# Kernel tuning notes

Measured on AMD Instinct MI355X. Metric: run time of the kernel, lower is better.

Reference implementation:

```python
import jax, jax.numpy as jnp
import numpy as np

NUM_HEADS = 16
THETA = 10000.0


def setup_inputs() -> dict:
    key = jax.random.key(0)
    k1, k2, k3, k4 = jax.random.split(key, 4)
    B, T, D = 2, 2048, 1024
    x = jax.random.normal(k1, (B, T, D), dtype=jnp.float32)
    token_positions = jnp.sort(
        jax.random.randint(k2, (B, T), 0, 2048), axis=-1
    ).astype(jnp.int32)
    sigma_qkv = float(np.sqrt(2.0 / (D + 3 * D)))
    sigma_out = float(np.sqrt(2.0 / (D + D)))
    W_qkv = jax.random.normal(k3, (3 * D, D), dtype=jnp.float32) * sigma_qkv
    W_out = jax.random.normal(k4, (D, D), dtype=jnp.float32) * sigma_out
    return {"x": x, "token_positions": token_positions, "W_qkv": W_qkv, "W_out": W_out}


def _apply_rope(t, cos, sin):
    # t: [B, H, T, d_k]; cos/sin: [B, T, d_k//2]
    B, H, T, dk = t.shape
    t2 = t.reshape(B, H, T, dk // 2, 2)
    te, to = t2[..., 0], t2[..., 1]
    c = cos[:, None]  # [B, 1, T, dk//2]
    s = sin[:, None]
    ye = te * c - to * s
    yo = to * c + te * s
    return jnp.stack([ye, yo], axis=-1).reshape(B, H, T, dk)


def reference(x, token_positions, W_qkv, W_out):
    B, T, D = x.shape
    H = NUM_HEADS
    dk = D // H

    # fused QKV projection: [B, T, 3D] -> split (three, h, d) on last dim
    qkv = jnp.einsum("btd,od->bto", x, W_qkv).reshape(B, T, 3, H, dk)
    qkv = jnp.transpose(qkv, (2, 0, 3, 1, 4))  # [3, B, H, T, dk]
    q, k, v = qkv[0], qkv[1], qkv[2]

    # RoPE angles from token positions
    n = jnp.arange(dk // 2, dtype=jnp.float32)
    inv_freq = THETA ** (-2.0 * n / dk)  # [dk//2]
    angles = token_positions.astype(jnp.float32)[..., None] * inv_freq  # [B, T, dk//2]
    cos, sin = jnp.cos(angles), jnp.sin(angles)
    q = _apply_rope(q, cos, sin)
    k = _apply_rope(k, cos, sin)

    # causal scaled dot-product attention
    scores = jnp.einsum("bhid,bhjd->bhij", q, k) / jnp.sqrt(jnp.float32(dk))
    causal = jnp.tril(jnp.ones((T, T), dtype=bool))
    scores = jnp.where(causal, scores, -jnp.inf)
    probs = jax.nn.softmax(scores, axis=-1)
    attn = jnp.einsum("bhij,bhjd->bhid", probs, v)  # [B, H, T, dk]

    concat = jnp.transpose(attn, (0, 2, 1, 3)).reshape(B, T, D)
    return jnp.einsum("btd,od->bto", concat, W_out)
```

## Files before the change

### kernel.cpp

```cpp
#include <hip/hip_runtime.h>
#include <hip/hip_bf16.h>
#include <cmath>

#define T_SEQ 2048
#define D_MODEL 1024
#define NHEAD 16
#define DK 64

typedef short bf16x8 __attribute__((ext_vector_type(8)));
typedef float f32x4 __attribute__((ext_vector_type(4)));
typedef float f32x16 __attribute__((ext_vector_type(16)));
typedef unsigned uint2v __attribute__((ext_vector_type(2)));

union U8 { unsigned u[4]; bf16x8 v; };

#define VMCNT(n) asm volatile("s_waitcnt vmcnt(" #n ")" ::: "memory")
#define BAR() __builtin_amdgcn_s_barrier()
#define SFENCE() __builtin_amdgcn_sched_barrier(0)

__device__ __forceinline__ short f2b(float f) {
    unsigned u = __builtin_bit_cast(unsigned, f);
    unsigned r = (u + 0x7FFFu + ((u >> 16) & 1u)) >> 16;
    return (short)r;
}

__device__ __forceinline__ void gll16(const void* g, void* l) {
    __builtin_amdgcn_global_load_lds(
        (__attribute__((address_space(1))) void*)g,
        (__attribute__((address_space(3))) void*)l, 16, 0, 0);
}

__device__ __forceinline__ bf16x8 lds_frag(const short* base, int row, int chunk) {
    return *reinterpret_cast<const bf16x8*>(
        (const char*)base + row * 128 + ((chunk * 16) ^ ((row & 7) << 4)));
}

__device__ __forceinline__ unsigned pkbf16(float a, float b) {
    unsigned r;
    asm("v_cvt_pk_bf16_f32 %0, %1, %2" : "=v"(r) : "v"(a), "v"(b));
    return r;
}
__device__ __forceinline__ void pl32swap(unsigned& a, unsigned& b) {
    uint2v r = __builtin_amdgcn_permlane32_swap(a, b, false, false);
    a = r.x; b = r.y;
}

__global__ __launch_bounds__(256) void cvt_all(const float* __restrict__ x,
                                               const float* __restrict__ wq,
                                               const float* __restrict__ wo,
                                               const int* __restrict__ pos,
                                               short* __restrict__ xb,
                                               short* __restrict__ wqb,
                                               short* __restrict__ wob,
                                               float* __restrict__ ct,
                                               float* __restrict__ st) {
    int i = blockIdx.x * 256 + threadIdx.x;
    if (i >= 1048576) {
        int j = i - 1048576;
        int bt = j >> 5, n = j & 31;
        float p = (float)pos[bt];
        float invf = expf((float)n * (-2.0f / (float)DK) * 9.210340371976184f);
        float s, c;
        sincosf(p * invf, &s, &c);
        ct[j] = c; st[j] = s;
        return;
    }
    const float* src;
    short* dst;
    int srcoff, c;
    if (i < 524288) {
        c = i;
        int tile = c >> 9, cc = c & 511;
        int kblk = cc >> 7, row = cc & 127;
        int rb = tile >> 5, kb = tile & 31;
        srcoff = (rb * 128 + row) * D_MODEL + kb * 32 + kblk * 8;
        src = x; dst = xb;
    } else if (i < 917504) {
        c = i - 524288;
        int tile = c >> 9, cc = c & 511;
        int kblk = cc >> 7, row = cc & 127;
        int rb = tile >> 5, kb = tile & 31;
        srcoff = (rb * 128 + row) * D_MODEL + kb * 32 + kblk * 8;
        src = wq; dst = wqb;
    } else {
        c = i - 917504;
        int tile = c >> 8, cc = c & 255;
        int kblk = cc >> 6, row = cc & 63;
        int nb = tile >> 5, kb = tile & 31;
        srcoff = (nb * 64 + row) * D_MODEL + kb * 32 + kblk * 8;
        src = wo; dst = wob;
    }
    float4 a = *reinterpret_cast<const float4*>(src + srcoff);
    float4 b = *reinterpret_cast<const float4*>(src + srcoff + 4);
    bf16x8 v;
    v[0] = f2b(a.x); v[1] = f2b(a.y); v[2] = f2b(a.z); v[3] = f2b(a.w);
    v[4] = f2b(b.x); v[5] = f2b(b.y); v[6] = f2b(b.z); v[7] = f2b(b.w);
    reinterpret_cast<bf16x8*>(dst)[c] = v;
}

__global__ __launch_bounds__(256, 3) void gemm_qkv(const short* __restrict__ xb,
                                                   const short* __restrict__ wb,
                                                   const float* __restrict__ ct,
                                                   const float* __restrict__ st,
                                                   short* __restrict__ Qo,
                                                   short* __restrict__ Ko,
                                                   short* __restrict__ Vt) {
    __shared__ short SM[3][8192];
    const int tid = threadIdx.x;
    const int w = tid >> 6, l = tid & 63, lg = l >> 4, li = l & 15;
    const int wr = w >> 1, wc = w & 1;
    const int bn = blockIdx.x * 128, bm = blockIdx.y * 128;

    const short* pA = xb + (size_t)blockIdx.y * 32 * 4096 + (w * 128 + l) * 8;
    const short* pB = wb + (size_t)blockIdx.x * 32 * 4096 + (w * 128 + l) * 8;

    f32x4 zero = {0.f, 0.f, 0.f, 0.f};
    f32x4 acc[4][4];
#pragma unroll
    for (int m = 0; m < 4; ++m)
#pragma unroll
        for (int n = 0; n < 4; ++n) acc[m][n] = zero;

#define GSTAGE(buf, t_)                                               \
    do {                                                              \
        const size_t ko = (size_t)(t_) * 4096;                        \
        gll16(pA + ko,       &SM[buf][w * 1024]);                     \
        gll16(pA + ko + 512, &SM[buf][w * 1024 + 512]);               \
        gll16(pB + ko,       &SM[buf][4096 + w * 1024]);              \
        gll16(pB + ko + 512, &SM[buf][4096 + w * 1024 + 512]);        \
    } while (0)

    GSTAGE(0, 0);
    GSTAGE(1, 1);

    for (int t = 0; t < 32; ++t) {
        if (t < 31) { VMCNT(4); } else { VMCNT(0); }
        BAR();
        SFENCE();
        if (t + 2 < 32) GSTAGE((t + 2) % 3, t + 2);
        const short* Ac = &SM[t % 3][0];
        const short* Bc = &SM[t % 3][4096];
        bf16x8 a[4], b[4];
#pragma unroll
        for (int m = 0; m < 4; ++m)
            a[m] = *reinterpret_cast<const bf16x8*>(&Ac[lg * 1024 + (wr * 64 + m * 16 + li) * 8]);
#pragma unroll
        for (int n = 0; n < 4; ++n)
            b[n] = *reinterpret_cast<const bf16x8*>(&Bc[lg * 1024 + (wc * 64 + n * 16 + li) * 8]);
        __builtin_amdgcn_s_setprio(1);
#pragma unroll
        for (int m = 0; m < 4; ++m)
#pragma unroll
            for (int n = 0; n < 4; ++n)
                acc[m][n] = __builtin_amdgcn_mfma_f32_16x16x32_bf16(a[m], b[n], acc[m][n], 0, 0, 0);
        __builtin_amdgcn_s_setprio(0);
    }
#undef GSTAGE

    const int which = bn >> 10;
    const int h = ((bn >> 6) + wc) & 15;
    if (which == 2) {
        __syncthreads();
        short* scr = &SM[0][0] + w * 4096;
#pragma unroll
        for (int n = 0; n < 4; ++n)
#pragma unroll
            for (int m = 0; m < 4; ++m)
#pragma unroll
                for (int rp = 0; rp < 2; ++rp) {
                    int d = n * 16 + li;
                    int t64 = m * 16 + lg * 4 + rp * 2;
                    unsigned pk = pkbf16(acc[m][n][rp * 2], acc[m][n][rp * 2 + 1]);
                    *reinterpret_cast<unsigned*>(
                        (char*)scr + ((d * 128 + t64 * 2) ^ ((d & 7) << 4))) = pk;
                }
        const int mi0 = bm + wr * 64;
        const int b0 = mi0 >> 11, t0 = mi0 & (T_SEQ - 1);
        short* vbase = Vt + (size_t)(b0 * NHEAD + h) * DK * T_SEQ + t0;
#pragma unroll
        for (int db = 0; db < 8; ++db) {
            int d = db * 8 + (l >> 3);
            int ch = l & 7;
            bf16x8 v = *reinterpret_cast<const bf16x8*>(
                (char*)scr + ((d * 128 + ch * 16) ^ ((d & 7) << 4)));
            *reinterpret_cast<bf16x8*>(vbase + (size_t)d * T_SEQ + ch * 8) = v;
        }
    } else {
#pragma unroll
        for (int n = 0; n < 4; ++n) {
            const int d = n * 16 + li;
#pragma unroll
            for (int m = 0; m < 4; ++m)
#pragma unroll
                for (int r = 0; r < 4; ++r) {
                    const int mi = bm + wr * 64 + m * 16 + lg * 4 + r;
                    const int b_ = mi >> 11, tt = mi & (T_SEQ - 1);
                    float v = acc[m][n][r];
                    float vp = __shfl_xor(v, 1);
                    int nn = n * 8 + (li >> 1);
                    float c = ct[(size_t)mi * 32 + nn];
                    float s = st[(size_t)mi * 32 + nn];
                    float o = (d & 1) ? (v * c + vp * s) : (v * c - vp * s);
                    if (which == 0) o *= 0.18033688011112042f;
                    short* dst = (which == 0) ? Qo : Ko;
                    dst[((size_t)((b_ * NHEAD + h) * T_SEQ + tt)) * DK + d] = f2b(o);
                }
        }
    }
}

__global__ __launch_bounds__(128, 3) void attn(const short* __restrict__ Q,
                                               const short* __restrict__ K,
                                               const short* __restrict__ Vt,
                                               short* __restrict__ Cc) {
    __shared__ short Kls[2][4096];

    const int bid = blockIdx.x;
    const int bh = bid & 31;
    const int qt = 31 - (bid >> 5);
    const int ntb = qt + 1;

    const int tid = threadIdx.x;
    const int w = tid >> 6, l = tid & 63;
    const int l31 = l & 31, hi = l >> 5, hi4 = hi * 4, hi8 = hi * 8;
    const int q0w = qt * 64 + w * 32;

    const short* Qh = Q + (size_t)bh * T_SEQ * DK;
    const short* Kh = K + (size_t)bh * T_SEQ * DK;
    const short* Vh = Vt + (size_t)bh * DK * T_SEQ;

    bf16x8 qf[4];
#pragma unroll
    for (int ks = 0; ks < 4; ++ks)
        qf[ks] = *reinterpret_cast<const bf16x8*>(&Qh[(size_t)(q0w + l31) * DK + ks * 16 + hi8]);

    f32x16 o0 = {0.f,0.f,0.f,0.f,0.f,0.f,0.f,0.f,0.f,0.f,0.f,0.f,0.f,0.f,0.f,0.f};
    f32x16 o1 = o0;
    float m = -3.0e38f;
    float lsum = 0.f;

    int rr[4], cb[4];
#pragma unroll
    for (int j = 0; j < 4; ++j) {
        int c = j * 128 + tid;
        rr[j] = c >> 3;
        cb[j] = ((c & 7) ^ (rr[j] & 7)) * 8;
    }
    auto kstage = [&](int buf, int n0_) {
#pragma unroll
        for (int j = 0; j < 4; ++j)
            gll16(Kh + (size_t)(n0_ + rr[j]) * DK + cb[j], &Kls[buf][j * 1024 + w * 512]);
    };

    const short* vrow0 = Vh + (size_t)l31 * T_SEQ;
    const short* vrow1 = Vh + (size_t)(32 + l31) * T_SEQ;

    kstage(0, 0);

    for (int t = 0; t < ntb; ++t) {
        VMCNT(0);
        BAR();
        const int n0 = t * 64;

        bf16x8 v00[2], v01[2], v10[2], v11[2];
#pragma unroll
        for (int kb = 0; kb < 2; ++kb) {
            const int co = n0 + (kb * 4 + hi) * 8;
            v00[kb] = *reinterpret_cast<const bf16x8*>(vrow0 + co);
            v01[kb] = *reinterpret_cast<const bf16x8*>(vrow0 + co + 16);
            v10[kb] = *reinterpret_cast<const bf16x8*>(vrow1 + co);
            v11[kb] = *reinterpret_cast<const bf16x8*>(vrow1 + co + 16);
        }
        if (t + 1 < ntb) kstage((t + 1) & 1, (t + 1) * 64);
        SFENCE();

        const short* Kc = Kls[t & 1];

        f32x16 s0 = {0.f,0.f,0.f,0.f,0.f,0.f,0.f,0.f,0.f,0.f,0.f,0.f,0.f,0.f,0.f,0.f};
        f32x16 s1 = s0;
        __builtin_amdgcn_s_setprio(1);
#pragma unroll
        for (int ks = 0; ks < 4; ++ks) {
            bf16x8 kf0 = lds_frag(Kc, l31,      ks * 2 + hi);
            bf16x8 kf1 = lds_frag(Kc, 32 + l31, ks * 2 + hi);
            s0 = __builtin_amdgcn_mfma_f32_32x32x16_bf16(kf0, qf[ks], s0, 0, 0, 0);
            s1 = __builtin_amdgcn_mfma_f32_32x32x16_bf16(kf1, qf[ks], s1, 0, 0, 0);
        }
        __builtin_amdgcn_s_setprio(0);

        float p[32];
#pragma unroll
        for (int r = 0; r < 16; ++r) { p[r] = s0[r]; p[16 + r] = s1[r]; }

        if (n0 + 64 > q0w) {
            const int qrel = q0w + l31 - n0;
#pragma unroll
            for (int r = 0; r < 16; ++r) {
                const int kvm = (r & 3) + 8 * (r >> 2) + hi4;
                if (kvm > qrel) p[r] = -3.0e38f;
                if (kvm + 32 > qrel) p[16 + r] = -3.0e38f;
            }
        }

        float t16[16];
#pragma unroll
        for (int r = 0; r < 16; ++r) t16[r] = fmaxf(p[r], p[16 + r]);
#pragma unroll
        for (int d = 8; d >= 1; d >>= 1)
#pragma unroll
            for (int r = 0; r < 8; ++r)
                if (r < d) t16[r] = fmaxf(t16[r], t16[r + d]);
        float tmax = fmaxf(t16[0], __shfl_xor(t16[0], 32));

        if (__any(tmax > m + 8.0f)) {
            float mnew = fmaxf(m, tmax);
            float alpha = __builtin_amdgcn_exp2f(m - mnew);
            m = mnew;
#pragma unroll
            for (int r = 0; r < 16; ++r) {
                float ar = __shfl(alpha, (r & 3) + 8 * (r >> 2) + hi4);
                o0[r] *= ar; o1[r] *= ar;
            }
            lsum *= alpha;
        }

#pragma unroll
        for (int r = 0; r < 32; ++r) p[r] = __builtin_amdgcn_exp2f(p[r] - m);
        float a16[16];
#pragma unroll
        for (int r = 0; r < 16; ++r) a16[r] = p[r] + p[16 + r];
#pragma unroll
        for (int d = 8; d >= 1; d >>= 1)
#pragma unroll
            for (int r = 0; r < 8; ++r)
                if (r < d) a16[r] += a16[r + d];
        lsum += a16[0] + __shfl_xor(a16[0], 32);

        __builtin_amdgcn_s_setprio(1);
#pragma unroll
        for (int kb = 0; kb < 2; ++kb) {
            unsigned pk0 = pkbf16(p[kb * 16 + 0],  p[kb * 16 + 1]);
            unsigned pk1 = pkbf16(p[kb * 16 + 2],  p[kb * 16 + 3]);
            unsigned pk2 = pkbf16(p[kb * 16 + 4],  p[kb * 16 + 5]);
            unsigned pk3 = pkbf16(p[kb * 16 + 6],  p[kb * 16 + 7]);
            unsigned pk4 = pkbf16(p[kb * 16 + 8],  p[kb * 16 + 9]);
            unsigned pk5 = pkbf16(p[kb * 16 + 10], p[kb * 16 + 11]);
            unsigned pk6 = pkbf16(p[kb * 16 + 12], p[kb * 16 + 13]);
            unsigned pk7 = pkbf16(p[kb * 16 + 14], p[kb * 16 + 15]);
            pl32swap(pk0, pk2); pl32swap(pk1, pk3);
            pl32swap(pk4, pk6); pl32swap(pk5, pk7);
            U8 f0, f1;
            f0.u[0] = pk0; f0.u[1] = pk1; f0.u[2] = pk2; f0.u[3] = pk3;
            f1.u[0] = pk4; f1.u[1] = pk5; f1.u[2] = pk6; f1.u[3] = pk7;
            o0 = __builtin_amdgcn_mfma_f32_32x32x16_bf16(f0.v, v00[kb], o0, 0, 0, 0);
            o0 = __builtin_amdgcn_mfma_f32_32x32x16_bf16(f1.v, v01[kb], o0, 0, 0, 0);
            o1 = __builtin_amdgcn_mfma_f32_32x32x16_bf16(f0.v, v10[kb], o1, 0, 0, 0);
            o1 = __builtin_amdgcn_mfma_f32_32x32x16_bf16(f1.v, v11[kb], o1, 0, 0, 0);
        }
        __builtin_amdgcn_s_setprio(0);
    }

    const int b = bh >> 4, h = bh & 15;
    const float linv = 1.0f / lsum;
#pragma unroll
    for (int r = 0; r < 16; ++r) {
        const int qoff = (r & 3) + 8 * (r >> 2) + hi4;
        float inv = __shfl(linv, qoff);
        const int mg = b * T_SEQ + q0w + qoff;
        const int mb = mg >> 7, row = mg & 127;
        const int kblk = l31 >> 3, el = l & 7;
        Cc[((size_t)(mb * 32 + h * 2 + 0)) * 4096 + kblk * 1024 + row * 8 + el] = f2b(o0[r] * inv);
        Cc[((size_t)(mb * 32 + h * 2 + 1)) * 4096 + kblk * 1024 + row * 8 + el] = f2b(o1[r] * inv);
    }
}

__global__ __launch_bounds__(256, 3) void gemm_out(const short* __restrict__ ab,
                                                   const short* __restrict__ wb,
                                                   float* __restrict__ out) {
    __shared__ short SM[3][6144];
    const int tid = threadIdx.x;
    const int w = tid >> 6, l = tid & 63, lg = l >> 4, li = l & 15;
    const int wr = w >> 1, wc = w & 1;
    const int bn = blockIdx.x * 64, bm = blockIdx.y * 128;

    const short* pA = ab + (size_t)blockIdx.y * 32 * 4096 + (w * 128 + l) * 8;
    const short* pB = wb + (size_t)blockIdx.x * 32 * 2048 + (w * 64 + l) * 8;

    f32x4 zero = {0.f, 0.f, 0.f, 0.f};
    f32x4 acc[4][2];
#pragma unroll
    for (int m = 0; m < 4; ++m)
#pragma unroll
        for (int n = 0; n < 2; ++n) acc[m][n] = zero;

#define OSTAGE(buf, t_)                                                  \
    do {                                                                 \
        gll16(pA + (size_t)(t_) * 4096,       &SM[buf][w * 1024]);       \
        gll16(pA + (size_t)(t_) * 4096 + 512, &SM[buf][w * 1024 + 512]); \
        gll16(pB + (size_t)(t_) * 2048,       &SM[buf][4096 + w * 512]); \
    } while (0)

    OSTAGE(0, 0);
    OSTAGE(1, 1);

    for (int t = 0; t < 32; ++t) {
        if (t < 31) { VMCNT(3); } else { VMCNT(0); }
        BAR();
        SFENCE();
        if (t + 2 < 32) OSTAGE((t + 2) % 3, t + 2);
        const short* Ac = &SM[t % 3][0];
        const short* Bc = &SM[t % 3][4096];
        bf16x8 a[4], b[2];
#pragma unroll
        for (int m = 0; m < 4; ++m)
            a[m] = *reinterpret_cast<const bf16x8*>(&Ac[lg * 1024 + (wr * 64 + m * 16 + li) * 8]);
#pragma unroll
        for (int n = 0; n < 2; ++n)
            b[n] = *reinterpret_cast<const bf16x8*>(&Bc[lg * 512 + (wc * 32 + n * 16 + li) * 8]);
        __builtin_amdgcn_s_setprio(1);
#pragma unroll
        for (int m = 0; m < 4; ++m)
#pragma unroll
            for (int n = 0; n < 2; ++n)
                acc[m][n] = __builtin_amdgcn_mfma_f32_16x16x32_bf16(a[m], b[n], acc[m][n], 0, 0, 0);
        __builtin_amdgcn_s_setprio(0);
    }
#undef OSTAGE

#pragma unroll
    for (int m = 0; m < 4; ++m)
#pragma unroll
        for (int n = 0; n < 2; ++n)
#pragma unroll
            for (int r = 0; r < 4; ++r) {
                const int mi = bm + wr * 64 + m * 16 + lg * 4 + r;
                out[(size_t)mi * D_MODEL + bn + wc * 32 + n * 16 + li] = acc[m][n][r];
            }
}

extern "C" void kernel_launch(void* const* d_in, const int* in_sizes, int n_in,
                              void* d_out, int out_size, void* d_ws, size_t ws_size,
                              hipStream_t stream) {
    const float* x    = (const float*)d_in[0];
    const int*   pos  = (const int*)d_in[1];
    const float* wqkv = (const float*)d_in[2];
    const float* wout = (const float*)d_in[3];
    float* out = (float*)d_out;

    char* ws = (char*)d_ws;
    size_t off = 0;
    short* xb  = (short*)(ws + off); off += (size_t)4096 * 1024 * 2;
    short* wqb = (short*)(ws + off); off += (size_t)3072 * 1024 * 2;
    short* wob = (short*)(ws + off); off += (size_t)1024 * 1024 * 2;
    short* Q   = (short*)(ws + off); off += (size_t)32 * 2048 * 64 * 2;
    short* Kb  = (short*)(ws + off); off += (size_t)32 * 2048 * 64 * 2;
    short* Vt  = (short*)(ws + off); off += (size_t)32 * 64 * 2048 * 2;
    off += 4096;
    short* Cc  = (short*)(ws + off); off += (size_t)4096 * 1024 * 2;
    float* ct  = (float*)(ws + off); off += (size_t)4096 * 32 * 4;
    float* st  = (float*)(ws + off); off += (size_t)4096 * 32 * 4;

    cvt_all<<<4608, 256, 0, stream>>>(x, wqkv, wout, pos, xb, wqb, wob, ct, st);
    gemm_qkv<<<dim3(24, 32), 256, 0, stream>>>(xb, wqb, ct, st, Q, Kb, Vt);
    attn<<<1024, 128, 0, stream>>>(Q, Kb, Vt, Cc);
    gemm_out<<<dim3(16, 32), 256, 0, stream>>>(Cc, wob, out);
}
```

Before: 127.3 us.

## Split causal attention over KV chunks with separate merge kernel and tiled V layout

Result: slower. 141.4 us (+11.1%).

```diff
diff --git a/kernel.cpp b/kernel.cpp
--- a/kernel.cpp
+++ b/kernel.cpp
@@ -22,6 +22,10 @@
     unsigned u = __builtin_bit_cast(unsigned, f);
     unsigned r = (u + 0x7FFFu + ((u >> 16) & 1u)) >> 16;
     return (short)r;
+}
+__device__ __forceinline__ float b2f(short s) {
+    unsigned u = ((unsigned)(unsigned short)s) << 16;
+    return __builtin_bit_cast(float, u);
 }
 
 __device__ __forceinline__ void gll16(const void* g, void* l) {
@@ -176,14 +180,15 @@
                 }
         const int mi0 = bm + wr * 64;
         const int b0 = mi0 >> 11, t0 = mi0 & (T_SEQ - 1);
-        short* vbase = Vt + (size_t)(b0 * NHEAD + h) * DK * T_SEQ + t0;
+        const int kvt = t0 >> 6;
+        short* vbase = Vt + ((size_t)(b0 * NHEAD + h) * 32 + kvt) * 4096;
+        const int ch = l >> 3;
 #pragma unroll
         for (int db = 0; db < 8; ++db) {
-            int d = db * 8 + (l >> 3);
-            int ch = l & 7;
+            int d = db * 8 + (l & 7);
             bf16x8 v = *reinterpret_cast<const bf16x8*>(
                 (char*)scr + ((d * 128 + ch * 16) ^ ((d & 7) << 4)));
-            *reinterpret_cast<bf16x8*>(vbase + (size_t)d * T_SEQ + ch * 8) = v;
+            *reinterpret_cast<bf16x8*>(vbase + ch * 512 + d * 8) = v;
         }
     } else {
 #pragma unroll
@@ -209,30 +214,37 @@
     }
 }
 
-__global__ __launch_bounds__(128, 3) void attn(const short* __restrict__ Q,
+__global__ __launch_bounds__(128, 4) void attn(const short* __restrict__ Q,
                                                const short* __restrict__ K,
                                                const short* __restrict__ Vt,
-                                               short* __restrict__ Cc) {
+                                               short* __restrict__ Cc,
+                                               short* __restrict__ Opart,
+                                               float* __restrict__ MLpart) {
     __shared__ short Kls[2][4096];
 
     const int bid = blockIdx.x;
     const int bh = bid & 31;
-    const int qt = 31 - (bid >> 5);
-    const int ntb = qt + 1;
+    const int rest = bid >> 5;
+    const int ch = rest & 3;
+    const int qt = 31 - (rest >> 2);
+    if (8 * ch > qt) return;
+    const int t0c = 8 * ch;
+    const int t1c = min(8 * ch + 8, qt + 1);
+    const int nch = (qt >> 3) + 1;
 
     const int tid = threadIdx.x;
     const int w = tid >> 6, l = tid & 63;
-    const int l31 = l & 31, hi = l >> 5, hi4 = hi * 4, hi8 = hi * 8;
+    const int l31 = l & 31, hi = l >> 5, hi4 = hi * 4;
     const int q0w = qt * 64 + w * 32;
 
     const short* Qh = Q + (size_t)bh * T_SEQ * DK;
     const short* Kh = K + (size_t)bh * T_SEQ * DK;
-    const short* Vh = Vt + (size_t)bh * DK * T_SEQ;
+    const short* Vh = Vt + (size_t)bh * 32 * 4096;
 
     bf16x8 qf[4];
 #pragma unroll
     for (int ks = 0; ks < 4; ++ks)
-        qf[ks] = *reinterpret_cast<const bf16x8*>(&Qh[(size_t)(q0w + l31) * DK + ks * 16 + hi8]);
+        qf[ks] = *reinterpret_cast<const bf16x8*>(&Qh[(size_t)(q0w + l31) * DK + ks * 16 + hi * 8]);
 
     f32x16 o0 = {0.f,0.f,0.f,0.f,0.f,0.f,0.f,0.f,0.f,0.f,0.f,0.f,0.f,0.f,0.f,0.f};
     f32x16 o1 = o0;
@@ -252,30 +264,26 @@
             gll16(Kh + (size_t)(n0_ + rr[j]) * DK + cb[j], &Kls[buf][j * 1024 + w * 512]);
     };
 
-    const short* vrow0 = Vh + (size_t)l31 * T_SEQ;
-    const short* vrow1 = Vh + (size_t)(32 + l31) * T_SEQ;
-
-    kstage(0, 0);
-
-    for (int t = 0; t < ntb; ++t) {
+    kstage(t0c & 1, t0c * 64);
+
+    for (int t = t0c; t < t1c; ++t) {
         VMCNT(0);
         BAR();
+        SFENCE();
         const int n0 = t * 64;
-
+        const short* vt = Vh + (size_t)t * 4096;
         bf16x8 v00[2], v01[2], v10[2], v11[2];
 #pragma unroll
         for (int kb = 0; kb < 2; ++kb) {
-            const int co = n0 + (kb * 4 + hi) * 8;
-            v00[kb] = *reinterpret_cast<const bf16x8*>(vrow0 + co);
-            v01[kb] = *reinterpret_cast<const bf16x8*>(vrow0 + co + 16);
-            v10[kb] = *reinterpret_cast<const bf16x8*>(vrow1 + co);
-            v11[kb] = *reinterpret_cast<const bf16x8*>(vrow1 + co + 16);
-        }
-        if (t + 1 < ntb) kstage((t + 1) & 1, (t + 1) * 64);
+            v00[kb] = *reinterpret_cast<const bf16x8*>(vt + (kb * 4 + hi) * 512 + l31 * 8);
+            v01[kb] = *reinterpret_cast<const bf16x8*>(vt + (kb * 4 + 2 + hi) * 512 + l31 * 8);
+            v10[kb] = *reinterpret_cast<const bf16x8*>(vt + (kb * 4 + hi) * 512 + 256 + l31 * 8);
+            v11[kb] = *reinterpret_cast<const bf16x8*>(vt + (kb * 4 + 2 + hi) * 512 + 256 + l31 * 8);
+        }
+        if (t + 1 < t1c) kstage((t + 1) & 1, (t + 1) * 64);
         SFENCE();
 
         const short* Kc = Kls[t & 1];
-
         f32x16 s0 = {0.f,0.f,0.f,0.f,0.f,0.f,0.f,0.f,0.f,0.f,0.f,0.f,0.f,0.f,0.f,0.f};
         f32x16 s1 = s0;
         __builtin_amdgcn_s_setprio(1);
@@ -360,18 +368,90 @@
         __builtin_amdgcn_s_setprio(0);
     }
 
+    if (nch == 1) {
+        const int b = bh >> 4, h = bh & 15;
+        const float linv = 1.0f / lsum;
+#pragma unroll
+        for (int r = 0; r < 16; ++r) {
+            const int qoff = (r & 3) + 8 * (r >> 2) + hi4;
+            float inv = __shfl(linv, qoff);
+            const int mg = b * T_SEQ + q0w + qoff;
+            const int mb = mg >> 7, row = mg & 127;
+            const int kblk = l31 >> 3, el = l & 7;
+            Cc[((size_t)(mb * 32 + h * 2 + 0)) * 4096 + kblk * 1024 + row * 8 + el] = f2b(o0[r] * inv);
+            Cc[((size_t)(mb * 32 + h * 2 + 1)) * 4096 + kblk * 1024 + row * 8 + el] = f2b(o1[r] * inv);
+        }
+    } else {
+        const int g = qt >> 3;
+        const int baseg = (g == 1) ? 0 : (g == 2) ? 16 : 40;
+        const int slot = bh * 72 + baseg + (g + 1) * (qt - g * 8) + ch;
+        short* op = Opart + (size_t)slot * 4096 + (w * 32) * 64;
+#pragma unroll
+        for (int r = 0; r < 16; ++r) {
+            const int qoff = (r & 3) + 8 * (r >> 2) + hi4;
+            op[qoff * 64 + l31]      = f2b(o0[r]);
+            op[qoff * 64 + 32 + l31] = f2b(o1[r]);
+        }
+        if (l < 32) {
+            float* mlp = MLpart + (size_t)slot * 128 + (w * 32 + l) * 2;
+            mlp[0] = m; mlp[1] = lsum;
+        }
+    }
+}
+
+__global__ __launch_bounds__(256) void attn_merge(const short* __restrict__ Opart,
+                                                  const float* __restrict__ MLpart,
+                                                  short* __restrict__ Cc) {
+    const int bid = blockIdx.x;
+    const int bh = bid & 31;
+    const int qt = 8 + (bid >> 5);
+    const int g = qt >> 3;
+    const int baseg = (g == 1) ? 0 : (g == 2) ? 16 : 40;
+    const int base = bh * 72 + baseg + (g + 1) * (qt - g * 8);
+    const int nch = g + 1;
+
+    const int tid = threadIdx.x;
+    const int q = tid >> 2, sl = tid & 3, d0 = sl * 16;
+
+    float mc[4], lc[4];
+    float M = -3.0e38f;
+    for (int c = 0; c < nch; ++c) {
+        const float* mlp = MLpart + (size_t)(base + c) * 128 + q * 2;
+        mc[c] = mlp[0]; lc[c] = mlp[1];
+        M = fmaxf(M, mc[c]);
+    }
+    float L = 0.f, al[4];
+    for (int c = 0; c < nch; ++c) {
+        al[c] = __builtin_amdgcn_exp2f(mc[c] - M);
+        L += al[c] * lc[c];
+    }
+    const float inv = 1.0f / L;
+
+    float acc[16];
+#pragma unroll
+    for (int e = 0; e < 16; ++e) acc[e] = 0.f;
+    for (int c = 0; c < nch; ++c) {
+        const short* src = Opart + (size_t)(base + c) * 4096 + q * 64 + d0;
+        bf16x8 v0 = *reinterpret_cast<const bf16x8*>(src);
+        bf16x8 v1 = *reinterpret_cast<const bf16x8*>(src + 8);
+#pragma unroll
+        for (int e = 0; e < 8; ++e) {
+            acc[e]     += al[c] * b2f(v0[e]);
+            acc[8 + e] += al[c] * b2f(v1[e]);
+        }
+    }
+
     const int b = bh >> 4, h = bh & 15;
-    const float linv = 1.0f / lsum;
-#pragma unroll
-    for (int r = 0; r < 16; ++r) {
-        const int qoff = (r & 3) + 8 * (r >> 2) + hi4;
-        float inv = __shfl(linv, qoff);
-        const int mg = b * T_SEQ + q0w + qoff;
-        const int mb = mg >> 7, row = mg & 127;
-        const int kblk = l31 >> 3, el = l & 7;
-        Cc[((size_t)(mb * 32 + h * 2 + 0)) * 4096 + kblk * 1024 + row * 8 + el] = f2b(o0[r] * inv);
-        Cc[((size_t)(mb * 32 + h * 2 + 1)) * 4096 + kblk * 1024 + row * 8 + el] = f2b(o1[r] * inv);
-    }
+    const int mg = b * T_SEQ + qt * 64 + q;
+    const int mb = mg >> 7, row = mg & 127;
+    short outv[16];
+#pragma unroll
+    for (int e = 0; e < 16; ++e) outv[e] = f2b(acc[e] * inv);
+    const int tile = mb * 32 + h * 2 + (d0 >> 5);
+    const int kb0 = (d0 & 31) >> 3;
+    short* dst = Cc + (size_t)tile * 4096 + kb0 * 1024 + row * 8;
+    *reinterpret_cast<bf16x8*>(dst)        = *reinterpret_cast<bf16x8*>(&outv[0]);
+    *reinterpret_cast<bf16x8*>(dst + 1024) = *reinterpret_cast<bf16x8*>(&outv[8]);
 }
 
 __global__ __launch_bounds__(256, 3) void gemm_out(const short* __restrict__ ab,
@@ -454,14 +534,17 @@
     short* wob = (short*)(ws + off); off += (size_t)1024 * 1024 * 2;
     short* Q   = (short*)(ws + off); off += (size_t)32 * 2048 * 64 * 2;
     short* Kb  = (short*)(ws + off); off += (size_t)32 * 2048 * 64 * 2;
-    short* Vt  = (short*)(ws + off); off += (size_t)32 * 64 * 2048 * 2;
+    short* Vt  = (short*)(ws + off); off += (size_t)32 * 32 * 4096 * 2;
     off += 4096;
     short* Cc  = (short*)(ws + off); off += (size_t)4096 * 1024 * 2;
     float* ct  = (float*)(ws + off); off += (size_t)4096 * 32 * 4;
     float* st  = (float*)(ws + off); off += (size_t)4096 * 32 * 4;
+    short* Opart = (short*)(ws + off); off += (size_t)2304 * 4096 * 2;
+    float* MLpart = (float*)(ws + off); off += (size_t)2304 * 128 * 4;
 
     cvt_all<<<4608, 256, 0, stream>>>(x, wqkv, wout, pos, xb, wqb, wob, ct, st);
     gemm_qkv<<<dim3(24, 32), 256, 0, stream>>>(xb, wqb, ct, st, Q, Kb, Vt);
-    attn<<<1024, 128, 0, stream>>>(Q, Kb, Vt, Cc);
+    attn<<<4096, 128, 0, stream>>>(Q, Kb, Vt, Cc, Opart, MLpart);
+    attn_merge<<<768, 256, 0, stream>>>(Opart, MLpart, Cc);
     gemm_out<<<dim3(16, 32), 256, 0, stream>>>(Cc, wob, out);
 }
```

## Pipeline PV MMA one tile behind, tile V per block, use 4-wave attention blocks

Applied to the files above, without the earlier changes.

New measurement: 112.9 us. 11.3% less time.

```diff
diff --git a/kernel.cpp b/kernel.cpp
--- a/kernel.cpp
+++ b/kernel.cpp
@@ -176,14 +176,15 @@
                 }
         const int mi0 = bm + wr * 64;
         const int b0 = mi0 >> 11, t0 = mi0 & (T_SEQ - 1);
-        short* vbase = Vt + (size_t)(b0 * NHEAD + h) * DK * T_SEQ + t0;
+        const int kvt = t0 >> 6;
+        short* vbase = Vt + ((size_t)(b0 * NHEAD + h) * 32 + kvt) * 4096;
+        const int ch = l >> 3;
 #pragma unroll
         for (int db = 0; db < 8; ++db) {
-            int d = db * 8 + (l >> 3);
-            int ch = l & 7;
+            int d = db * 8 + (l & 7);
             bf16x8 v = *reinterpret_cast<const bf16x8*>(
                 (char*)scr + ((d * 128 + ch * 16) ^ ((d & 7) << 4)));
-            *reinterpret_cast<bf16x8*>(vbase + (size_t)d * T_SEQ + ch * 8) = v;
+            *reinterpret_cast<bf16x8*>(vbase + ch * 512 + d * 8) = v;
         }
     } else {
 #pragma unroll
@@ -209,25 +210,27 @@
     }
 }
 
-__global__ __launch_bounds__(128, 3) void attn(const short* __restrict__ Q,
+__global__ __launch_bounds__(256, 3) void attn(const short* __restrict__ Q,
                                                const short* __restrict__ K,
                                                const short* __restrict__ Vt,
                                                short* __restrict__ Cc) {
     __shared__ short Kls[2][4096];
 
     const int bid = blockIdx.x;
-    const int bh = bid & 31;
-    const int qt = 31 - (bid >> 5);
-    const int ntb = qt + 1;
+    const int ii = bid & 255, rhalf = bid >> 8;
+    const int bh = ii & 31;
+    const int qt = rhalf ? 15 - (ii >> 5) : (ii >> 5);
+    const int ntb = 2 * qt + 2;
 
     const int tid = threadIdx.x;
     const int w = tid >> 6, l = tid & 63;
     const int l31 = l & 31, hi = l >> 5, hi4 = hi * 4, hi8 = hi * 8;
-    const int q0w = qt * 64 + w * 32;
+    const int q0w = qt * 128 + w * 32;
+    const int Tw = (q0w + 32 + 63) >> 6;
 
     const short* Qh = Q + (size_t)bh * T_SEQ * DK;
     const short* Kh = K + (size_t)bh * T_SEQ * DK;
-    const short* Vh = Vt + (size_t)bh * DK * T_SEQ;
+    const short* Vh = Vt + (size_t)bh * 32 * 4096;
 
     bf16x8 qf[4];
 #pragma unroll
@@ -239,126 +242,137 @@
     float m = -3.0e38f;
     float lsum = 0.f;
 
-    int rr[4], cb[4];
-#pragma unroll
-    for (int j = 0; j < 4; ++j) {
-        int c = j * 128 + tid;
-        rr[j] = c >> 3;
-        cb[j] = ((c & 7) ^ (rr[j] & 7)) * 8;
+    int kr0, kc0, kr1, kc1;
+    {
+        int c0 = tid;        kr0 = c0 >> 3; kc0 = ((c0 & 7) ^ (kr0 & 7)) * 8;
+        int c1 = 256 + tid;  kr1 = c1 >> 3; kc1 = ((c1 & 7) ^ (kr1 & 7)) * 8;
     }
     auto kstage = [&](int buf, int n0_) {
-#pragma unroll
-        for (int j = 0; j < 4; ++j)
-            gll16(Kh + (size_t)(n0_ + rr[j]) * DK + cb[j], &Kls[buf][j * 1024 + w * 512]);
+        gll16(Kh + (size_t)(n0_ + kr0) * DK + kc0, &Kls[buf][w * 512]);
+        gll16(Kh + (size_t)(n0_ + kr1) * DK + kc1, &Kls[buf][2048 + w * 512]);
     };
 
-    const short* vrow0 = Vh + (size_t)l31 * T_SEQ;
-    const short* vrow1 = Vh + (size_t)(32 + l31) * T_SEQ;
+    bf16x8 v00[2], v01[2], v10[2], v11[2];
+    U8 pf0[2], pf1[2];
 
     kstage(0, 0);
 
     for (int t = 0; t < ntb; ++t) {
         VMCNT(0);
         BAR();
-        const int n0 = t * 64;
-
-        bf16x8 v00[2], v01[2], v10[2], v11[2];
-#pragma unroll
-        for (int kb = 0; kb < 2; ++kb) {
-            const int co = n0 + (kb * 4 + hi) * 8;
-            v00[kb] = *reinterpret_cast<const bf16x8*>(vrow0 + co);
-            v01[kb] = *reinterpret_cast<const bf16x8*>(vrow0 + co + 16);
-            v10[kb] = *reinterpret_cast<const bf16x8*>(vrow1 + co);
-            v11[kb] = *reinterpret_cast<const bf16x8*>(vrow1 + co + 16);
+        SFENCE();
+        if (t + 1 < ntb) kstage((t + 1) & 1, (t + 1) * 64);
+
+        if (t < Tw) {
+            const int n0 = t * 64;
+            const short* Kc = Kls[t & 1];
+
+            f32x16 s0 = {0.f,0.f,0.f,0.f,0.f,0.f,0.f,0.f,0.f,0.f,0.f,0.f,0.f,0.f,0.f,0.f};
+            f32x16 s1 = s0;
+            __builtin_amdgcn_s_setprio(1);
+#pragma unroll
+            for (int ks = 0; ks < 4; ++ks) {
+                bf16x8 kf0 = lds_frag(Kc, l31,      ks * 2 + hi);
+                bf16x8 kf1 = lds_frag(Kc, 32 + l31, ks * 2 + hi);
+                s0 = __builtin_amdgcn_mfma_f32_32x32x16_bf16(kf0, qf[ks], s0, 0, 0, 0);
+                s1 = __builtin_amdgcn_mfma_f32_32x32x16_bf16(kf1, qf[ks], s1, 0, 0, 0);
+            }
+            if (t > 0) {
+#pragma unroll
+                for (int kb = 0; kb < 2; ++kb) {
+                    o0 = __builtin_amdgcn_mfma_f32_32x32x16_bf16(pf0[kb].v, v00[kb], o0, 0, 0, 0);
+                    o0 = __builtin_amdgcn_mfma_f32_32x32x16_bf16(pf1[kb].v, v01[kb], o0, 0, 0, 0);
+                    o1 = __builtin_amdgcn_mfma_f32_32x32x16_bf16(pf0[kb].v, v10[kb], o1, 0, 0, 0);
+                    o1 = __builtin_amdgcn_mfma_f32_32x32x16_bf16(pf1[kb].v, v11[kb], o1, 0, 0, 0);
+                }
+            }
+            __builtin_amdgcn_s_setprio(0);
+
+            const short* vt = Vh + (size_t)t * 4096;
+#pragma unroll
+            for (int kb = 0; kb < 2; ++kb) {
+                v00[kb] = *reinterpret_cast<const bf16x8*>(vt + (kb * 4 + hi) * 512 + l31 * 8);
+                v01[kb] = *reinterpret_cast<const bf16x8*>(vt + (kb * 4 + 2 + hi) * 512 + l31 * 8);
+                v10[kb] = *reinterpret_cast<const bf16x8*>(vt + (kb * 4 + hi) * 512 + 256 + l31 * 8);
+                v11[kb] = *reinterpret_cast<const bf16x8*>(vt + (kb * 4 + 2 + hi) * 512 + 256 + l31 * 8);
+            }
+            SFENCE();
+
+            float p[32];
+#pragma unroll
+            for (int r = 0; r < 16; ++r) { p[r] = s0[r]; p[16 + r] = s1[r]; }
+
+            if (n0 + 64 > q0w) {
+                const int qrel = q0w + l31 - n0;
+#pragma unroll
+                for (int r = 0; r < 16; ++r) {
+                    const int kvm = (r & 3) + 8 * (r >> 2) + hi4;
+                    if (kvm > qrel) p[r] = -3.0e38f;
+                    if (kvm + 32 > qrel) p[16 + r] = -3.0e38f;
+                }
+            }
+
+            float t16[16];
+#pragma unroll
+            for (int r = 0; r < 16; ++r) t16[r] = fmaxf(p[r], p[16 + r]);
+#pragma unroll
+            for (int d = 8; d >= 1; d >>= 1)
+#pragma unroll
+                for (int r = 0; r < 8; ++r)
+                    if (r < d) t16[r] = fmaxf(t16[r], t16[r + d]);
+            float tmax = fmaxf(t16[0], __shfl_xor(t16[0], 32));
+
+            if (__any(tmax > m + 8.0f)) {
+                float mnew = fmaxf(m, tmax);
+                float alpha = __builtin_amdgcn_exp2f(m - mnew);
+                m = mnew;
+#pragma unroll
+                for (int r = 0; r < 16; ++r) {
+                    float ar = __shfl(alpha, (r & 3) + 8 * (r >> 2) + hi4);
+                    o0[r] *= ar; o1[r] *= ar;
+                }
+                lsum *= alpha;
+            }
+
+#pragma unroll
+            for (int r = 0; r < 32; ++r) p[r] = __builtin_amdgcn_exp2f(p[r] - m);
+            float a16[16];
+#pragma unroll
+            for (int r = 0; r < 16; ++r) a16[r] = p[r] + p[16 + r];
+#pragma unroll
+            for (int d = 8; d >= 1; d >>= 1)
+#pragma unroll
+                for (int r = 0; r < 8; ++r)
+                    if (r < d) a16[r] += a16[r + d];
+            lsum += a16[0] + __shfl_xor(a16[0], 32);
+
+#pragma unroll
+            for (int kb = 0; kb < 2; ++kb) {
+                unsigned pk0 = pkbf16(p[kb * 16 + 0],  p[kb * 16 + 1]);
+                unsigned pk1 = pkbf16(p[kb * 16 + 2],  p[kb * 16 + 3]);
+                unsigned pk2 = pkbf16(p[kb * 16 + 4],  p[kb * 16 + 5]);
+                unsigned pk3 = pkbf16(p[kb * 16 + 6],  p[kb * 16 + 7]);
+                unsigned pk4 = pkbf16(p[kb * 16 + 8],  p[kb * 16 + 9]);
+                unsigned pk5 = pkbf16(p[kb * 16 + 10], p[kb * 16 + 11]);
+                unsigned pk6 = pkbf16(p[kb * 16 + 12], p[kb * 16 + 13]);
+                unsigned pk7 = pkbf16(p[kb * 16 + 14], p[kb * 16 + 15]);
+                pl32swap(pk0, pk2); pl32swap(pk1, pk3);
+                pl32swap(pk4, pk6); pl32swap(pk5, pk7);
+                pf0[kb].u[0] = pk0; pf0[kb].u[1] = pk1; pf0[kb].u[2] = pk2; pf0[kb].u[3] = pk3;
+                pf1[kb].u[0] = pk4; pf1[kb].u[1] = pk5; pf1[kb].u[2] = pk6; pf1[kb].u[3] = pk7;
+            }
         }
-        if (t + 1 < ntb) kstage((t + 1) & 1, (t + 1) * 64);
-        SFENCE();
-
-        const short* Kc = Kls[t & 1];
-
-        f32x16 s0 = {0.f,0.f,0.f,0.f,0.f,0.f,0.f,0.f,0.f,0.f,0.f,0.f,0.f,0.f,0.f,0.f};
-        f32x16 s1 = s0;
-        __builtin_amdgcn_s_setprio(1);
-#pragma unroll
-        for (int ks = 0; ks < 4; ++ks) {
-            bf16x8 kf0 = lds_frag(Kc, l31,      ks * 2 + hi);
-            bf16x8 kf1 = lds_frag(Kc, 32 + l31, ks * 2 + hi);
-            s0 = __builtin_amdgcn_mfma_f32_32x32x16_bf16(kf0, qf[ks], s0, 0, 0, 0);
-            s1 = __builtin_amdgcn_mfma_f32_32x32x16_bf16(kf1, qf[ks], s1, 0, 0, 0);
-        }
-        __builtin_amdgcn_s_setprio(0);
-
-        float p[32];
-#pragma unroll
-        for (int r = 0; r < 16; ++r) { p[r] = s0[r]; p[16 + r] = s1[r]; }
-
-        if (n0 + 64 > q0w) {
-            const int qrel = q0w + l31 - n0;
-#pragma unroll
-            for (int r = 0; r < 16; ++r) {
-                const int kvm = (r & 3) + 8 * (r >> 2) + hi4;
-                if (kvm > qrel) p[r] = -3.0e38f;
-                if (kvm + 32 > qrel) p[16 + r] = -3.0e38f;
-            }
-        }
-
-        float t16[16];
-#pragma unroll
-        for (int r = 0; r < 16; ++r) t16[r] = fmaxf(p[r], p[16 + r]);
-#pragma unroll
-        for (int d = 8; d >= 1; d >>= 1)
-#pragma unroll
-            for (int r = 0; r < 8; ++r)
-                if (r < d) t16[r] = fmaxf(t16[r], t16[r + d]);
-        float tmax = fmaxf(t16[0], __shfl_xor(t16[0], 32));
-
-        if (__any(tmax > m + 8.0f)) {
-            float mnew = fmaxf(m, tmax);
-            float alpha = __builtin_amdgcn_exp2f(m - mnew);
-            m = mnew;
-#pragma unroll
-            for (int r = 0; r < 16; ++r) {
-                float ar = __shfl(alpha, (r & 3) + 8 * (r >> 2) + hi4);
-                o0[r] *= ar; o1[r] *= ar;
-            }
-            lsum *= alpha;
-        }
-
-#pragma unroll
-        for (int r = 0; r < 32; ++r) p[r] = __builtin_amdgcn_exp2f(p[r] - m);
-        float a16[16];
-#pragma unroll
-        for (int r = 0; r < 16; ++r) a16[r] = p[r] + p[16 + r];
-#pragma unroll
-        for (int d = 8; d >= 1; d >>= 1)
-#pragma unroll
-            for (int r = 0; r < 8; ++r)
-                if (r < d) a16[r] += a16[r + d];
-        lsum += a16[0] + __shfl_xor(a16[0], 32);
-
-        __builtin_amdgcn_s_setprio(1);
-#pragma unroll
-        for (int kb = 0; kb < 2; ++kb) {
-            unsigned pk0 = pkbf16(p[kb * 16 + 0],  p[kb * 16 + 1]);
-            unsigned pk1 = pkbf16(p[kb * 16 + 2],  p[kb * 16 + 3]);
-            unsigned pk2 = pkbf16(p[kb * 16 + 4],  p[kb * 16 + 5]);
-            unsigned pk3 = pkbf16(p[kb * 16 + 6],  p[kb * 16 + 7]);
-            unsigned pk4 = pkbf16(p[kb * 16 + 8],  p[kb * 16 + 9]);
-            unsigned pk5 = pkbf16(p[kb * 16 + 10], p[kb * 16 + 11]);
-            unsigned pk6 = pkbf16(p[kb * 16 + 12], p[kb * 16 + 13]);
-            unsigned pk7 = pkbf16(p[kb * 16 + 14], p[kb * 16 + 15]);
-            pl32swap(pk0, pk2); pl32swap(pk1, pk3);
-            pl32swap(pk4, pk6); pl32swap(pk5, pk7);
-            U8 f0, f1;
-            f0.u[0] = pk0; f0.u[1] = pk1; f0.u[2] = pk2; f0.u[3] = pk3;
-            f1.u[0] = pk4; f1.u[1] = pk5; f1.u[2] = pk6; f1.u[3] = pk7;
-            o0 = __builtin_amdgcn_mfma_f32_32x32x16_bf16(f0.v, v00[kb], o0, 0, 0, 0);
-            o0 = __builtin_amdgcn_mfma_f32_32x32x16_bf16(f1.v, v01[kb], o0, 0, 0, 0);
-            o1 = __builtin_amdgcn_mfma_f32_32x32x16_bf16(f0.v, v10[kb], o1, 0, 0, 0);
-            o1 = __builtin_amdgcn_mfma_f32_32x32x16_bf16(f1.v, v11[kb], o1, 0, 0, 0);
-        }
-        __builtin_amdgcn_s_setprio(0);
-    }
+    }
+
+    __builtin_amdgcn_s_setprio(1);
+#pragma unroll
+    for (int kb = 0; kb < 2; ++kb) {
+        o0 = __builtin_amdgcn_mfma_f32_32x32x16_bf16(pf0[kb].v, v00[kb], o0, 0, 0, 0);
+        o0 = __builtin_amdgcn_mfma_f32_32x32x16_bf16(pf1[kb].v, v01[kb], o0, 0, 0, 0);
+        o1 = __builtin_amdgcn_mfma_f32_32x32x16_bf16(pf0[kb].v, v10[kb], o1, 0, 0, 0);
+        o1 = __builtin_amdgcn_mfma_f32_32x32x16_bf16(pf1[kb].v, v11[kb], o1, 0, 0, 0);
+    }
+    __builtin_amdgcn_s_setprio(0);
 
     const int b = bh >> 4, h = bh & 15;
     const float linv = 1.0f / lsum;
@@ -454,7 +468,7 @@
     short* wob = (short*)(ws + off); off += (size_t)1024 * 1024 * 2;
     short* Q   = (short*)(ws + off); off += (size_t)32 * 2048 * 64 * 2;
     short* Kb  = (short*)(ws + off); off += (size_t)32 * 2048 * 64 * 2;
-    short* Vt  = (short*)(ws + off); off += (size_t)32 * 64 * 2048 * 2;
+    short* Vt  = (short*)(ws + off); off += (size_t)32 * 32 * 4096 * 2;
     off += 4096;
     short* Cc  = (short*)(ws + off); off += (size_t)4096 * 1024 * 2;
     float* ct  = (float*)(ws + off); off += (size_t)4096 * 32 * 4;
@@ -462,6 +476,6 @@
 
     cvt_all<<<4608, 256, 0, stream>>>(x, wqkv, wout, pos, xb, wqb, wob, ct, st);
     gemm_qkv<<<dim3(24, 32), 256, 0, stream>>>(xb, wqb, ct, st, Q, Kb, Vt);
-    attn<<<1024, 128, 0, stream>>>(Q, Kb, Vt, Cc);
+    attn<<<512, 256, 0, stream>>>(Q, Kb, Vt, Cc);
     gemm_out<<<dim3(16, 32), 256, 0, stream>>>(Cc, wob, out);
 }
```
